# Performance work log

Hardware: AMD Instinct MI355X
Metric: run time of the kernel (lower is better)

## Reference

```python
import jax, jax.numpy as jnp
import numpy as np

D0 = 1.0          # constraint distance d
NPEND = 128       # points per pendulum chain
NB = 1024         # number of chains (= batch.max()+1)
LATENT = 256      # latent dim of y
NDIM = 3          # spatial dimensions; x dim = 2*NDIM (pos + vel)


def setup_inputs() -> dict:
    key = jax.random.key(0)
    k1, k2, k3 = jax.random.split(key, 3)
    N = NB * NPEND
    y = jax.random.normal(k1, (N, LATENT), dtype=jnp.float32)
    z = jax.random.normal(k2, (N,), dtype=jnp.float32)
    K = jax.random.normal(k3, (LATENT, 2 * NDIM), dtype=jnp.float32) * 0.05
    batch = (jnp.arange(N, dtype=jnp.int32) // NPEND).astype(jnp.int32)
    return {"y": y, "z": z, "K": K, "batch": batch}


def _delta_r(r):
    # dr[:,0] = r[:,0]; dr[:,i] = r[:,i] - r[:,i-1]
    return jnp.concatenate([r[:, :1], r[:, 1:] - r[:, :-1]], axis=1)


def reference(y, z, K, batch):
    x = y @ K                                  # [N, 6]
    ndim = x.shape[-1] // 2                    # pos_only=False -> 3
    nb = batch.shape[0] // NPEND               # == batch.max()+1 by construction
    r = x[:, :ndim].reshape(nb, -1, ndim)      # [nb, npend, 3]

    dr = _delta_r(r)                           # [nb, npend, 3]
    drnorm = jnp.linalg.norm(dr, axis=-1)      # [nb, npend]
    c = drnorm - D0                            # constraint values
    rn = dr / drnorm[..., None]                # unit chain-difference vectors

    # Jacobian-transpose times constraints, fused over the chain dimension:
    # out[:,i] = c_i * rn_i - c_{i+1} * rn_{i+1};  out[:,-1] = c_{-1} * rn_{-1}
    t = c[..., None] * rn                      # [nb, npend, 3]
    out = t - jnp.concatenate([t[:, 1:], jnp.zeros_like(t[:, :1])], axis=1)

    lam_x = jnp.zeros_like(x).at[:, :ndim].set(out.reshape(-1, ndim))
    lam_y = lam_x @ K.T                        # [N, latent]
    return lam_y
```

## Files before the change

### kernel.cpp

```cpp
#include <hip/hip_runtime.h>

#define NPEND  128
#define LATENT 256
#define KCOLS  6
#define D0_C   1.0f
#define NB_MAX 1024

typedef float f32x4 __attribute__((ext_vector_type(4)));

__global__ __launch_bounds__(256, 2)
void pend_fused_kernel(const float* __restrict__ y,
                       const float* __restrict__ K,
                       float* __restrict__ out)
{
    __shared__ float4 sR[NPEND];

    const int tid = threadIdx.x;
    const int sl  = tid & 15;
    const int grp = tid >> 4;
    const int hl  = tid & 31;
    const int hw  = tid >> 5;
    const int l0  = hl * 4;

    const int chain = blockIdx.x;
    const float* ybase = y   + (size_t)chain * (NPEND * LATENT);
    float*       obase = out + (size_t)chain * (NPEND * LATENT);

    float4 b0[4], b1[4];

    auto issueA = [&](int i, float4 (&b)[4]) {
        const float* p = ybase + (grp * 8 + i) * LATENT + sl * 4;
        b[0] = *(const float4*)(p);
        b[1] = *(const float4*)(p + 64);
        b[2] = *(const float4*)(p + 128);
        b[3] = *(const float4*)(p + 192);
    };

    issueA(0, b0);

    float kf0[16], kf1[16], kf2[16];
#pragma unroll
    for (int j = 0; j < 4; ++j)
#pragma unroll
        for (int e = 0; e < 4; ++e) {
            const int k = j * 64 + sl * 4 + e;
            kf0[4 * j + e] = K[k * KCOLS + 0];
            kf1[4 * j + e] = K[k * KCOLS + 1];
            kf2[4 * j + e] = K[k * KCOLS + 2];
        }
    float ka[8], kb[8], kc[8];
#pragma unroll
    for (int e = 0; e < 4; ++e) {
        ka[e]     = K[(l0 + e) * KCOLS + 0];
        kb[e]     = K[(l0 + e) * KCOLS + 1];
        kc[e]     = K[(l0 + e) * KCOLS + 2];
        ka[4 + e] = K[(l0 + 128 + e) * KCOLS + 0];
        kb[4 + e] = K[(l0 + 128 + e) * KCOLS + 1];
        kc[4 + e] = K[(l0 + 128 + e) * KCOLS + 2];
    }

    auto consumeA = [&](int i, const float4 (&b)[4]) {
        float s0 = 0.f, s1 = 0.f, s2 = 0.f;
#pragma unroll
        for (int j = 0; j < 4; ++j) {
            const float4 a = b[j];
            s0 += a.x*kf0[4*j] + a.y*kf0[4*j+1] + a.z*kf0[4*j+2] + a.w*kf0[4*j+3];
            s1 += a.x*kf1[4*j] + a.y*kf1[4*j+1] + a.z*kf1[4*j+2] + a.w*kf1[4*j+3];
            s2 += a.x*kf2[4*j] + a.y*kf2[4*j+1] + a.z*kf2[4*j+2] + a.w*kf2[4*j+3];
        }
#pragma unroll
        for (int off = 8; off >= 1; off >>= 1) {
            s0 += __shfl_xor(s0, off, 16);
            s1 += __shfl_xor(s1, off, 16);
            s2 += __shfl_xor(s2, off, 16);
        }
        if (sl == 0) sR[grp * 8 + i] = make_float4(s0, s1, s2, 0.f);
    };

    __builtin_amdgcn_sched_barrier(0);
    issueA(1, b1);
    __builtin_amdgcn_sched_barrier(0);
    consumeA(0, b0);
    issueA(2, b0);
    __builtin_amdgcn_sched_barrier(0);
    consumeA(1, b1);
    issueA(3, b1);
    __builtin_amdgcn_sched_barrier(0);
    consumeA(2, b0);
    issueA(4, b0);
    __builtin_amdgcn_sched_barrier(0);
    consumeA(3, b1);
    issueA(5, b1);
    __builtin_amdgcn_sched_barrier(0);
    consumeA(4, b0);
    issueA(6, b0);
    __builtin_amdgcn_sched_barrier(0);
    consumeA(5, b1);
    issueA(7, b1);
    __builtin_amdgcn_sched_barrier(0);
    consumeA(6, b0);
    consumeA(7, b1);

    __syncthreads();

    const int r0 = hw * 16;
    float4 rc = sR[r0];
    float4 rp = (r0 > 0) ? sR[r0 - 1] : make_float4(0.f, 0.f, 0.f, 0.f);

#pragma unroll
    for (int i = 0; i < 16; ++i) {
        const int row = r0 + i;
        const float4 rn = sR[(row < NPEND - 1) ? row + 1 : row];

        const float dx = rc.x - rp.x, dy = rc.y - rp.y, dz = rc.z - rp.z;
        const float n  = sqrtf(dx*dx + dy*dy + dz*dz);
        const float s  = (n - D0_C) / n;
        float ox = s * dx, oy = s * dy, oz = s * dz;

        if (row < NPEND - 1) {
            const float ex = rn.x - rc.x, ey = rn.y - rc.y, ez = rn.z - rc.z;
            const float n2 = sqrtf(ex*ex + ey*ey + ez*ez);
            const float t2 = (n2 - D0_C) / n2;
            ox -= t2 * ex; oy -= t2 * ey; oz -= t2 * ez;
        }

        f32x4 wa, wb;
        wa.x = ox*ka[0] + oy*kb[0] + oz*kc[0];
        wa.y = ox*ka[1] + oy*kb[1] + oz*kc[1];
        wa.z = ox*ka[2] + oy*kb[2] + oz*kc[2];
        wa.w = ox*ka[3] + oy*kb[3] + oz*kc[3];
        wb.x = ox*ka[4] + oy*kb[4] + oz*kc[4];
        wb.y = ox*ka[5] + oy*kb[5] + oz*kc[5];
        wb.z = ox*ka[6] + oy*kb[6] + oz*kc[6];
        wb.w = ox*ka[7] + oy*kb[7] + oz*kc[7];

        float* orow = obase + (size_t)row * LATENT;
        __builtin_nontemporal_store(wa, (f32x4*)(orow + l0));
        __builtin_nontemporal_store(wb, (f32x4*)(orow + 128 + l0));

        rp = rc; rc = rn;
    }
}

extern "C" void kernel_launch(void* const* d_in, const int* in_sizes, int n_in,
                              void* d_out, int out_size, void* d_ws, size_t ws_size,
                              hipStream_t stream) {
    const float* y = (const float*)d_in[0];
    const float* K = (const float*)d_in[2];
    float* out = (float*)d_out;

    int N  = (n_in > 1 && in_sizes) ? in_sizes[1] : (1024 * NPEND);
    int nb = N / NPEND;
    if (nb <= 0) nb = 1024;
    if (nb > NB_MAX) nb = NB_MAX;
    (void)out_size; (void)d_ws; (void)ws_size;

    pend_fused_kernel<<<nb, 256, 0, stream>>>(y, K, out);
}
```

Before: 235.9 us.

## Split each chain across two half-blocks with a one-row halo

Each pendulum chain is now handled by two 128-thread blocks, each covering 64 rows. The grid doubles to 2048 blocks so more waves are in flight to hide memory latency. Each half loads one extra y row as a halo for the neighbouring difference, so a small amount of projection work is recomputed. The transposed-K register loads move after the barrier to shorten their live range, and the nontemporal output stores become plain vector stores, which changes cache behaviour on the write stream.

```diff
diff --git a/kernel.cpp b/kernel.cpp
--- a/kernel.cpp
+++ b/kernel.cpp
@@ -8,12 +8,12 @@
 
 typedef float f32x4 __attribute__((ext_vector_type(4)));
 
-__global__ __launch_bounds__(256, 2)
+__global__ __launch_bounds__(128, 4)
 void pend_fused_kernel(const float* __restrict__ y,
                        const float* __restrict__ K,
                        float* __restrict__ out)
 {
-    __shared__ float4 sR[NPEND];
+    __shared__ float4 sR[65];
 
     const int tid = threadIdx.x;
     const int sl  = tid & 15;
@@ -22,14 +22,18 @@
     const int hw  = tid >> 5;
     const int l0  = hl * 4;
 
-    const int chain = blockIdx.x;
+    const int chain = blockIdx.x >> 1;
+    const int half  = blockIdx.x & 1;
+    const int r0    = half << 6;
+    const int rbase = r0 - half;
+
     const float* ybase = y   + (size_t)chain * (NPEND * LATENT);
     float*       obase = out + (size_t)chain * (NPEND * LATENT);
 
     float4 b0[4], b1[4];
 
     auto issueA = [&](int i, float4 (&b)[4]) {
-        const float* p = ybase + (grp * 8 + i) * LATENT + sl * 4;
+        const float* p = ybase + (rbase + grp * 8 + i) * LATENT + sl * 4;
         b[0] = *(const float4*)(p);
         b[1] = *(const float4*)(p + 64);
         b[2] = *(const float4*)(p + 128);
@@ -48,16 +52,6 @@
             kf1[4 * j + e] = K[k * KCOLS + 1];
             kf2[4 * j + e] = K[k * KCOLS + 2];
         }
-    float ka[8], kb[8], kc[8];
-#pragma unroll
-    for (int e = 0; e < 4; ++e) {
-        ka[e]     = K[(l0 + e) * KCOLS + 0];
-        kb[e]     = K[(l0 + e) * KCOLS + 1];
-        kc[e]     = K[(l0 + e) * KCOLS + 2];
-        ka[4 + e] = K[(l0 + 128 + e) * KCOLS + 0];
-        kb[4 + e] = K[(l0 + 128 + e) * KCOLS + 1];
-        kc[4 + e] = K[(l0 + 128 + e) * KCOLS + 2];
-    }
 
     auto consumeA = [&](int i, const float4 (&b)[4]) {
         float s0 = 0.f, s1 = 0.f, s2 = 0.f;
@@ -80,37 +74,47 @@
     __builtin_amdgcn_sched_barrier(0);
     issueA(1, b1);
     __builtin_amdgcn_sched_barrier(0);
-    consumeA(0, b0);
-    issueA(2, b0);
+    consumeA(0, b0); issueA(2, b0);
     __builtin_amdgcn_sched_barrier(0);
-    consumeA(1, b1);
-    issueA(3, b1);
+    consumeA(1, b1); issueA(3, b1);
     __builtin_amdgcn_sched_barrier(0);
-    consumeA(2, b0);
-    issueA(4, b0);
+    consumeA(2, b0); issueA(4, b0);
     __builtin_amdgcn_sched_barrier(0);
-    consumeA(3, b1);
-    issueA(5, b1);
+    consumeA(3, b1); issueA(5, b1);
     __builtin_amdgcn_sched_barrier(0);
-    consumeA(4, b0);
-    issueA(6, b0);
+    consumeA(4, b0); issueA(6, b0);
     __builtin_amdgcn_sched_barrier(0);
-    consumeA(5, b1);
-    issueA(7, b1);
+    consumeA(5, b1); issueA(7, b1);
     __builtin_amdgcn_sched_barrier(0);
     consumeA(6, b0);
+    if (grp == 7) issueA(8, b0);
+    __builtin_amdgcn_sched_barrier(0);
     consumeA(7, b1);
+    __builtin_amdgcn_sched_barrier(0);
+    if (grp == 7) consumeA(8, b0);
 
     __syncthreads();
 
-    const int r0 = hw * 16;
-    float4 rc = sR[r0];
-    float4 rp = (r0 > 0) ? sR[r0 - 1] : make_float4(0.f, 0.f, 0.f, 0.f);
+    float ka[8], kb[8], kc[8];
+#pragma unroll
+    for (int e = 0; e < 4; ++e) {
+        ka[e]     = K[(l0 + e) * KCOLS + 0];
+        kb[e]     = K[(l0 + e) * KCOLS + 1];
+        kc[e]     = K[(l0 + e) * KCOLS + 2];
+        ka[4 + e] = K[(l0 + 128 + e) * KCOLS + 0];
+        kb[4 + e] = K[(l0 + 128 + e) * KCOLS + 1];
+        kc[4 + e] = K[(l0 + 128 + e) * KCOLS + 2];
+    }
+
+    const int li0 = (r0 - rbase) + hw * 16;
+    float4 rc = sR[li0];
+    float4 rp = (r0 + hw * 16 > 0) ? sR[li0 - 1] : make_float4(0.f, 0.f, 0.f, 0.f);
 
 #pragma unroll
     for (int i = 0; i < 16; ++i) {
-        const int row = r0 + i;
-        const float4 rn = sR[(row < NPEND - 1) ? row + 1 : row];
+        const int row = r0 + hw * 16 + i;
+        const int li  = li0 + i;
+        const float4 rn = sR[(row < NPEND - 1) ? li + 1 : li];
 
         const float dx = rc.x - rp.x, dy = rc.y - rp.y, dz = rc.z - rp.z;
         const float n  = sqrtf(dx*dx + dy*dy + dz*dz);
@@ -124,7 +128,7 @@
             ox -= t2 * ex; oy -= t2 * ey; oz -= t2 * ez;
         }
 
-        f32x4 wa, wb;
+        float4 wa, wb;
         wa.x = ox*ka[0] + oy*kb[0] + oz*kc[0];
         wa.y = ox*ka[1] + oy*kb[1] + oz*kc[1];
         wa.z = ox*ka[2] + oy*kb[2] + oz*kc[2];
@@ -135,8 +139,8 @@
         wb.w = ox*ka[7] + oy*kb[7] + oz*kc[7];
 
         float* orow = obase + (size_t)row * LATENT;
-        __builtin_nontemporal_store(wa, (f32x4*)(orow + l0));
-        __builtin_nontemporal_store(wb, (f32x4*)(orow + 128 + l0));
+        *(float4*)(orow + l0)       = wa;
+        *(float4*)(orow + 128 + l0) = wb;
 
         rp = rc; rc = rn;
     }
@@ -155,5 +159,5 @@
     if (nb > NB_MAX) nb = NB_MAX;
     (void)out_size; (void)d_ws; (void)ws_size;
 
-    pend_fused_kernel<<<nb, 256, 0, stream>>>(y, K, out);
+    pend_fused_kernel<<<nb * 2, 128, 0, stream>>>(y, K, out);
 }
```

Measured after the change: 240.2 us. About the same (+1.8%).
